# Kernel optimization log

Measured on AMD Instinct MI355X. Metric: run time of the kernel, lower is better.

Reference implementation:

```python
import jax, jax.numpy as jnp
from jax import lax
import numpy as np

B, T, I, H, L, O = 64, 256, 128, 1024, 3, 2


def setup_inputs() -> dict:
    key = jax.random.key(0)
    ks = jax.random.split(key, 12)
    std = 1.0 / np.sqrt(H)
    u = lambda k, shape: jax.random.uniform(k, shape, jnp.float32, -std, std)
    return {
        "x": jax.random.normal(ks[0], (B, T, I), jnp.float32),
        # layer 0 cell (input_size -> hidden)
        "wx0": u(ks[1], (H, I)), "bx0": u(ks[2], (H,)),
        "wh0": u(ks[3], (H, H)), "bh0": u(ks[4], (H,)),
        # layers 1..L-1 cells (hidden -> hidden), stacked
        "wx": u(ks[5], (L - 1, H, H)), "bx": u(ks[6], (L - 1, H)),
        "wh": u(ks[7], (L - 1, H, H)), "bh": u(ks[8], (L - 1, H)),
        # final fc
        "fcw": u(ks[9], (O, H)), "fcb": u(ks[10], (O,)),
    }


def reference(x, wx0, bx0, wh0, bh0, wx, bx, wh, bh, fcw, fcb):
    b = x.shape[0]
    n_rest = wx.shape[0]  # num_layers - 1
    h0 = jnp.zeros((n_rest + 1, b, wh0.shape[0]), x.dtype)
    xT = jnp.swapaxes(x, 0, 1)  # [T, B, I]

    def step(hs, xt):
        new = []
        h = jnp.tanh(xt @ wx0.T + bx0 + hs[0] @ wh0.T + bh0)
        new.append(h)
        for l in range(n_rest):  # small fixed layer loop
            h = jnp.tanh(new[l] @ wx[l].T + bx[l] + hs[l + 1] @ wh[l].T + bh[l])
            new.append(h)
        return jnp.stack(new), None

    hs_final, _ = lax.scan(step, h0, xT)
    # original collects per-step top-layer outputs but only uses the last one
    return hs_final[-1] @ fcw.T + fcb  # [B, O]
```

## Files before the change

### kernel.cpp

```cpp
#include <hip/hip_runtime.h>


typedef __attribute__((ext_vector_type(8))) short short8;
typedef __attribute__((ext_vector_type(4))) float float4v;

#define DEVFN static __device__ __forceinline__

#define GLD(dst, ptr) \
  asm volatile("global_load_dwordx4 %0, %1, off sc1" : "=v"(dst) : "v"(ptr))
#define GST16(ptr, val) \
  asm volatile("global_store_dwordx4 %0, %1, off sc1" :: "v"(ptr), "v"(val) : "memory")
#define GDRAIN() do { asm volatile("s_waitcnt vmcnt(0)" ::: "memory"); \
                      __builtin_amdgcn_sched_barrier(0); } while (0)

DEVFN unsigned short f2bf(float f) {
  unsigned int u = __float_as_uint(f);
  u += 0x7FFFu + ((u >> 16) & 1u);
  return (unsigned short)(u >> 16);
}
DEVFN float bf2f(unsigned short h) { return __uint_as_float(((unsigned int)h) << 16); }

DEVFN void spin_ge(int* p, int want) {
  while (__hip_atomic_load(p, __ATOMIC_RELAXED, __HIP_MEMORY_SCOPE_AGENT) < want)
    __builtin_amdgcn_s_sleep(1);
}

namespace rnncfg {
constexpr int  TT = 256, HH = 1024;
constexpr long WELEMS = 1024L * 1152 + 2L * 1024 * 2048;
constexpr long XELEMS = 64L * 256 * 128;
constexpr long HELEMS = 3L * 4 * 64 * HH;
constexpr long PELEMS = 48L * 4 * 4096;

constexpr long OFF_WHI  = 0;
constexpr long OFF_WLO  = OFF_WHI + WELEMS * 2;
constexpr long OFF_XHI  = OFF_WLO + WELEMS * 2;
constexpr long OFF_XLO  = OFF_XHI + XELEMS * 2;
constexpr long OFF_HHI  = OFF_XLO + XELEMS * 2;
constexpr long OFF_HLO  = OFF_HHI + HELEMS * 2;
constexpr long OFF_BIAS = OFF_HLO + HELEMS * 2;
constexpr long OFF_CNT  = OFF_BIAS + 3L * HH * 4;
constexpr long N_CNT    = 768 + 48L * 256;
constexpr long OFF_PART = OFF_CNT + N_CNT * 4;
constexpr long WS_NEED  = OFF_PART + PELEMS * 4;

constexpr int SMEM_BYTES = 4 * 64 * 65 * 4;
}

__global__ __launch_bounds__(256) void rnn_prep_kernel(
    const float* __restrict__ x,
    const float* __restrict__ wx0, const float* __restrict__ bx0,
    const float* __restrict__ wh0, const float* __restrict__ bh0,
    const float* __restrict__ wx,  const float* __restrict__ bx,
    const float* __restrict__ wh,  const float* __restrict__ bh,
    char* __restrict__ ws)
{
  using namespace rnncfg;
  unsigned short* WHI = (unsigned short*)(ws + OFF_WHI);
  unsigned short* WLO = (unsigned short*)(ws + OFF_WLO);
  unsigned short* XHI = (unsigned short*)(ws + OFF_XHI);
  unsigned short* XLO = (unsigned short*)(ws + OFF_XLO);
  float* BIAS = (float*)(ws + OFF_BIAS);
  int*   CNT  = (int*)(ws + OFF_CNT);
  const long i0 = (long)blockIdx.x * blockDim.x + threadIdx.x;
  const long st = (long)gridDim.x * blockDim.x;

  for (long i = i0; i < N_CNT; i += st) CNT[i] = 0;

  for (long i = i0; i < 3 * HH; i += st) {
    int l = (int)(i >> 10), n = (int)(i & 1023);
    BIAS[i] = (l == 0) ? (bx0[n] + bh0[n]) : (bx[(l - 1) * HH + n] + bh[(l - 1) * HH + n]);
  }
  for (long i = i0; i < XELEMS; i += st) {
    float v = x[i];
    unsigned short h = f2bf(v);
    XHI[i] = h; XLO[i] = f2bf(v - bf2f(h));
  }
  for (long i = i0; i < WELEMS; i += st) {
    long j = i; int n, k; float v;
    if (j < 1179648L) {
      n = (int)(j / 1152); k = (int)(j % 1152);
      v = (k < 128) ? wx0[n * 128 + k] : wh0[(long)n * 1024 + (k - 128)];
    } else if (j < 3276800L) {
      j -= 1179648L; n = (int)(j / 2048); k = (int)(j % 2048);
      v = (k < 1024) ? wx[(long)n * 1024 + k] : wh[(long)n * 1024 + (k - 1024)];
    } else {
      j -= 3276800L; n = (int)(j / 2048); k = (int)(j % 2048);
      v = (k < 1024) ? wx[1048576L + (long)n * 1024 + k]
                     : wh[1048576L + (long)n * 1024 + (k - 1024)];
    }
    unsigned short h = f2bf(v);
    WHI[i] = h; WLO[i] = f2bf(v - bf2f(h));
  }
}

#define MFMA(a, b, c) __builtin_amdgcn_mfma_f32_16x16x32_bf16((a), (b), (c), 0, 0, 0)

template<int L>
DEVFN void run_block(char* __restrict__ ws, int tid, int g, int cg, int q,
                     float* __restrict__ pbuf, int* __restrict__ sFlag)
{
  using namespace rnncfg;
  constexpr long LWOFF = (L == 0) ? 0L : ((L == 1) ? 1179648L : 3276800L);
  constexpr int  KL    = (L == 0) ? 1152 : 2048;

  const unsigned short* WHI = (const unsigned short*)(ws + OFF_WHI);
  const unsigned short* WLO = (const unsigned short*)(ws + OFF_WLO);
  const unsigned short* XHI = (const unsigned short*)(ws + OFF_XHI);
  const unsigned short* XLO = (const unsigned short*)(ws + OFF_XLO);
  unsigned short* HHI = (unsigned short*)(ws + OFF_HHI);
  unsigned short* HLO = (unsigned short*)(ws + OFF_HLO);
  const float* BIAS = (const float*)(ws + OFF_BIAS);
  int* READY = (int*)(ws + OFF_CNT);
  int* ARR   = READY + 768;
  float* PART = (float*)(ws + OFF_PART);

  const int lane = tid & 63, wv = tid >> 6;
  const int rowb = lane & 15;
  const int kof  = (lane >> 4) * 8;
  const int n0   = cg * 64;

  short8 bh[4][4], bl[4][4];
  short8 bxh[4], bxl[4];
  if constexpr (L == 0) {
#pragma unroll
    for (int nt = 0; nt < 4; ++nt) {
      const long wr = LWOFF + (long)(n0 + nt * 16 + rowb) * KL;
      if (q == 0) { bxh[nt] = *(const short8*)(WHI + wr + wv * 32 + kof);
                    bxl[nt] = *(const short8*)(WLO + wr + wv * 32 + kof); }
#pragma unroll
      for (int j = 0; j < 2; ++j) {
        const int kc = 128 + q * 256 + wv * 64 + j * 32 + kof;
        bh[nt][j] = *(const short8*)(WHI + wr + kc);
        bl[nt][j] = *(const short8*)(WLO + wr + kc);
      }
    }
  } else {
#pragma unroll
    for (int nt = 0; nt < 4; ++nt) {
      const long wr = LWOFF + (long)(n0 + nt * 16 + rowb) * KL;
#pragma unroll
      for (int ks = 0; ks < 4; ++ks) {
        const int kc = q * 512 + wv * 128 + ks * 32 + kof;
        bh[nt][ks] = *(const short8*)(WHI + wr + kc);
        bl[nt][ks] = *(const short8*)(WLO + wr + kc);
      }
    }
  }

  float* myP = PART + (long)(g * 4 + q) * 4096;
  int* arrp = ARR + g * 256;

  for (int t = 0; t < TT; ++t) {
    if (tid == 0) {
      if (t > 0) spin_ge(&READY[L * 256 + t - 1], 16);
      if (L > 0) spin_ge(&READY[(L - 1) * 256 + t], 16);
    }
    __syncthreads();

    const unsigned short* selfH = HHI + (long)(L * 4 + ((t - 1) & 3)) * 65536;
    const unsigned short* selfL = HLO + (long)(L * 4 + ((t - 1) & 3)) * 65536;

    float4v acc[4][4];
#pragma unroll
    for (int mt = 0; mt < 4; ++mt)
#pragma unroll
      for (int nt = 0; nt < 4; ++nt) acc[mt][nt] = (float4v){0.f, 0.f, 0.f, 0.f};

    if constexpr (L == 0) {
      short8 xh[4], xl[4], ah[4][2], al[4][2];
      if (q == 0) {
#pragma unroll
        for (int mt = 0; mt < 4; ++mt) {
          const long xo = ((long)(mt * 16 + rowb) * 256 + t) * 128 + wv * 32 + kof;
          xh[mt] = *(const short8*)(XHI + xo);
          xl[mt] = *(const short8*)(XLO + xo);
        }
      }
      if (t > 0) {
        const int kb = q * 256 + wv * 64 + kof;
#pragma unroll
        for (int mt = 0; mt < 4; ++mt) {
          const int ao = (mt * 16 + rowb) * 1024 + kb;
#pragma unroll
          for (int j = 0; j < 2; ++j) { GLD(ah[mt][j], selfH + ao + j * 32);
                                        GLD(al[mt][j], selfL + ao + j * 32); }
        }
      }
      GDRAIN();
      if (q == 0) {
#pragma unroll
        for (int mt = 0; mt < 4; ++mt)
#pragma unroll
          for (int nt = 0; nt < 4; ++nt) {
            acc[mt][nt] = MFMA(xh[mt], bxh[nt], acc[mt][nt]);
            acc[mt][nt] = MFMA(xh[mt], bxl[nt], acc[mt][nt]);
            acc[mt][nt] = MFMA(xl[mt], bxh[nt], acc[mt][nt]);
          }
      }
      if (t > 0) {
#pragma unroll
        for (int j = 0; j < 2; ++j)
#pragma unroll
          for (int mt = 0; mt < 4; ++mt)
#pragma unroll
            for (int nt = 0; nt < 4; ++nt) {
              acc[mt][nt] = MFMA(ah[mt][j], bh[nt][j], acc[mt][nt]);
              acc[mt][nt] = MFMA(ah[mt][j], bl[nt][j], acc[mt][nt]);
              acc[mt][nt] = MFMA(al[mt][j], bh[nt][j], acc[mt][nt]);
            }
      }
    } else {
      if (!(t == 0 && q >= 2)) {
        const unsigned short* AH = (q < 2)
            ? HHI + (long)((L - 1) * 4 + (t & 3)) * 65536 : selfH;
        const unsigned short* AL = (q < 2)
            ? HLO + (long)((L - 1) * 4 + (t & 3)) * 65536 : selfL;
        const int kb = (q & 1) * 512 + wv * 128 + kof;
        short8 ah[4][4], al[4][4];
#pragma unroll
        for (int mt = 0; mt < 4; ++mt) {
          const int ao = (mt * 16 + rowb) * 1024 + kb;
#pragma unroll
          for (int ks = 0; ks < 4; ++ks) { GLD(ah[mt][ks], AH + ao + ks * 32);
                                           GLD(al[mt][ks], AL + ao + ks * 32); }
        }
        GDRAIN();
#pragma unroll
        for (int ks = 0; ks < 4; ++ks)
#pragma unroll
          for (int mt = 0; mt < 4; ++mt)
#pragma unroll
            for (int nt = 0; nt < 4; ++nt) {
              acc[mt][nt] = MFMA(ah[mt][ks], bh[nt][ks], acc[mt][nt]);
              acc[mt][nt] = MFMA(ah[mt][ks], bl[nt][ks], acc[mt][nt]);
              acc[mt][nt] = MFMA(al[mt][ks], bh[nt][ks], acc[mt][nt]);
            }
      }
    }

#pragma unroll
    for (int mt = 0; mt < 4; ++mt)
#pragma unroll
      for (int nt = 0; nt < 4; ++nt)
#pragma unroll
        for (int r = 0; r < 4; ++r)
          pbuf[wv * 4160 + (mt * 16 + (lane >> 4) * 4 + r) * 65 + nt * 16 + rowb]
              = acc[mt][nt][r];
    __syncthreads();

    {
      const int prow = tid >> 2, pc0 = (tid & 3) * 16;
#pragma unroll
      for (int cq = 0; cq < 4; ++cq) {
        float4v s = *(const float4v*)(pbuf +        prow * 65 + pc0 + cq * 4);
        s += *(const float4v*)(pbuf + 4160 + prow * 65 + pc0 + cq * 4);
        s += *(const float4v*)(pbuf + 8320 + prow * 65 + pc0 + cq * 4);
        s += *(const float4v*)(pbuf + 12480 + prow * 65 + pc0 + cq * 4);
        GST16(myP + prow * 64 + pc0 + cq * 4, s);
      }
    }
    GDRAIN();
    __syncthreads();
    if (tid == 0) {
      const int old = __hip_atomic_fetch_add(&arrp[t], 1, __ATOMIC_RELAXED,
                                             __HIP_MEMORY_SCOPE_AGENT);
      *sFlag = (old == 3);
    }
    __syncthreads();

    if (*sFlag) {
      if (tid == 0 && L < 2 && t >= 4) spin_ge(&READY[(L + 1) * 256 + t - 4], 16);
      __syncthreads();

      const int prow = tid >> 2, pc0 = (tid & 3) * 16;
      const float* P0 = PART + (long)(g * 4) * 4096 + prow * 64 + pc0;
      float4v pa[4][4];
#pragma unroll
      for (int qq = 0; qq < 4; ++qq)
#pragma unroll
        for (int cq = 0; cq < 4; ++cq)
          GLD(pa[qq][cq], P0 + qq * 4096 + cq * 4);
      GDRAIN();

      unsigned short* dH = HHI + (long)(L * 4 + (t & 3)) * 65536 + prow * 1024 + n0 + pc0;
      unsigned short* dL = HLO + (long)(L * 4 + (t & 3)) * 65536 + prow * 1024 + n0 + pc0;
      short8 vh[2], vl[2];
#pragma unroll
      for (int cq = 0; cq < 4; ++cq) {
        const float4v s = (pa[0][cq] + pa[1][cq]) + (pa[2][cq] + pa[3][cq]);
#pragma unroll
        for (int j = 0; j < 4; ++j) {
          const float v = tanhf(s[j] + BIAS[L * 1024 + n0 + pc0 + cq * 4 + j]);
          const unsigned short hh = f2bf(v);
          vh[cq >> 1][(cq & 1) * 4 + j] = (short)hh;
          vl[cq >> 1][(cq & 1) * 4 + j] = (short)f2bf(v - bf2f(hh));
        }
      }
      GST16(dH, vh[0]); GST16(dH + 8, vh[1]);
      GST16(dL, vl[0]); GST16(dL + 8, vl[1]);
      GDRAIN();
      __syncthreads();
      if (tid == 0)
        __hip_atomic_fetch_add(&READY[L * 256 + t], 1, __ATOMIC_RELAXED,
                               __HIP_MEMORY_SCOPE_AGENT);
    }
  }
}

__global__ __launch_bounds__(256, 1) void rnn_pipeline_kernel(
    char* __restrict__ ws, const float* __restrict__ fcw,
    const float* __restrict__ fcb, float* __restrict__ out)
{
  using namespace rnncfg;
  extern __shared__ float pbuf[];
  __shared__ int sFlag;
  const int tid = threadIdx.x, bid = blockIdx.x;

  const int xcd = bid & 7, s = bid >> 3;
  const int q = s & 3, gslot = s >> 2;
  const int g = gslot * 8 + xcd;
  const int layer = g >> 4, cg = g & 15;

  if (layer == 0)      run_block<0>(ws, tid, g, cg, q, pbuf, &sFlag);
  else if (layer == 1) run_block<1>(ws, tid, g, cg, q, pbuf, &sFlag);
  else                 run_block<2>(ws, tid, g, cg, q, pbuf, &sFlag);

  if (bid == 0) {
    int* READY = (int*)(ws + OFF_CNT);
    if (tid == 0) spin_ge(&READY[2 * 256 + 255], 16);
    __syncthreads();
    if (tid < 128) {
      const unsigned short* HHI = (const unsigned short*)(ws + OFF_HHI);
      const unsigned short* HLO = (const unsigned short*)(ws + OFF_HLO);
      const int bb = tid >> 1, o = tid & 1;
      const unsigned short* hH = HHI + (long)(2 * 4 + 3) * 65536 + (long)bb * 1024;
      const unsigned short* hL = HLO + (long)(2 * 4 + 3) * 65536 + (long)bb * 1024;
      const float* w = fcw + o * 1024;
      float sum = fcb[o];
      for (int n = 0; n < 1024; n += 32) {
        short8 vh[4], vl[4];
#pragma unroll
        for (int qq = 0; qq < 4; ++qq) { GLD(vh[qq], hH + n + qq * 8);
                                         GLD(vl[qq], hL + n + qq * 8); }
        GDRAIN();
#pragma unroll
        for (int qq = 0; qq < 4; ++qq)
#pragma unroll
          for (int j = 0; j < 8; ++j)
            sum += (bf2f((unsigned short)vh[qq][j]) + bf2f((unsigned short)vl[qq][j]))
                   * w[n + qq * 8 + j];
      }
      out[bb * 2 + o] = sum;
    }
  }
}

extern "C" void kernel_launch(void* const* d_in, const int* in_sizes, int n_in,
                              void* d_out, int out_size, void* d_ws, size_t ws_size,
                              hipStream_t stream)
{
  using namespace rnncfg;
  const float* x   = (const float*)d_in[0];
  const float* wx0 = (const float*)d_in[1];
  const float* bx0 = (const float*)d_in[2];
  const float* wh0 = (const float*)d_in[3];
  const float* bh0 = (const float*)d_in[4];
  const float* wx  = (const float*)d_in[5];
  const float* bx  = (const float*)d_in[6];
  const float* wh  = (const float*)d_in[7];
  const float* bh  = (const float*)d_in[8];
  const float* fcw = (const float*)d_in[9];
  const float* fcb = (const float*)d_in[10];
  char* ws = (char*)d_ws;
  float* out = (float*)d_out;

  if (ws_size < (size_t)WS_NEED) return;

  hipFuncSetAttribute(reinterpret_cast<const void*>(rnn_pipeline_kernel),
                      hipFuncAttributeMaxDynamicSharedMemorySize, SMEM_BYTES);

  rnn_prep_kernel<<<dim3(1024), dim3(256), 0, stream>>>(
      x, wx0, bx0, wh0, bh0, wx, bx, wh, bh, ws);
  rnn_pipeline_kernel<<<dim3(192), dim3(256), SMEM_BYTES, stream>>>(
      ws, fcw, fcb, out);
}
```

Measured before the change: 4.128 ms.

## Replace per-layer step barriers with fine-grained per-column-group ready flags

```diff
diff --git a/kernel.cpp b/kernel.cpp
--- a/kernel.cpp
+++ b/kernel.cpp
@@ -23,6 +23,16 @@
 DEVFN void spin_ge(int* p, int want) {
   while (__hip_atomic_load(p, __ATOMIC_RELAXED, __HIP_MEMORY_SCOPE_AGENT) < want)
     __builtin_amdgcn_s_sleep(1);
+}
+
+DEVFN void spin_flags(int* base, int n) {
+  const int tid = threadIdx.x;
+  if (tid < n) {
+    int* p = base + tid;
+    while (__hip_atomic_load(p, __ATOMIC_RELAXED, __HIP_MEMORY_SCOPE_AGENT) < 1)
+      __builtin_amdgcn_s_sleep(1);
+  }
+  __syncthreads();
 }
 
 namespace rnncfg {
@@ -40,7 +50,7 @@
 constexpr long OFF_HLO  = OFF_HHI + HELEMS * 2;
 constexpr long OFF_BIAS = OFF_HLO + HELEMS * 2;
 constexpr long OFF_CNT  = OFF_BIAS + 3L * HH * 4;
-constexpr long N_CNT    = 768 + 48L * 256;
+constexpr long N_CNT    = 768 + 48L * 256 + 3L * 256 * 16;
 constexpr long OFF_PART = OFF_CNT + N_CNT * 4;
 constexpr long WS_NEED  = OFF_PART + PELEMS * 4;
 
@@ -111,8 +121,9 @@
   unsigned short* HHI = (unsigned short*)(ws + OFF_HHI);
   unsigned short* HLO = (unsigned short*)(ws + OFF_HLO);
   const float* BIAS = (const float*)(ws + OFF_BIAS);
-  int* READY = (int*)(ws + OFF_CNT);
-  int* ARR   = READY + 768;
+  int* READY  = (int*)(ws + OFF_CNT);
+  int* ARR    = READY + 768;
+  int* READY2 = ARR + 48 * 256;
   float* PART = (float*)(ws + OFF_PART);
 
   const int lane = tid & 63, wv = tid >> 6;
@@ -152,15 +163,6 @@
   int* arrp = ARR + g * 256;
 
   for (int t = 0; t < TT; ++t) {
-    if (tid == 0) {
-      if (t > 0) spin_ge(&READY[L * 256 + t - 1], 16);
-      if (L > 0) spin_ge(&READY[(L - 1) * 256 + t], 16);
-    }
-    __syncthreads();
-
-    const unsigned short* selfH = HHI + (long)(L * 4 + ((t - 1) & 3)) * 65536;
-    const unsigned short* selfL = HLO + (long)(L * 4 + ((t - 1) & 3)) * 65536;
-
     float4v acc[4][4];
 #pragma unroll
     for (int mt = 0; mt < 4; ++mt)
@@ -168,27 +170,14 @@
       for (int nt = 0; nt < 4; ++nt) acc[mt][nt] = (float4v){0.f, 0.f, 0.f, 0.f};
 
     if constexpr (L == 0) {
-      short8 xh[4], xl[4], ah[4][2], al[4][2];
       if (q == 0) {
+        short8 xh[4], xl[4];
 #pragma unroll
         for (int mt = 0; mt < 4; ++mt) {
           const long xo = ((long)(mt * 16 + rowb) * 256 + t) * 128 + wv * 32 + kof;
           xh[mt] = *(const short8*)(XHI + xo);
           xl[mt] = *(const short8*)(XLO + xo);
         }
-      }
-      if (t > 0) {
-        const int kb = q * 256 + wv * 64 + kof;
-#pragma unroll
-        for (int mt = 0; mt < 4; ++mt) {
-          const int ao = (mt * 16 + rowb) * 1024 + kb;
-#pragma unroll
-          for (int j = 0; j < 2; ++j) { GLD(ah[mt][j], selfH + ao + j * 32);
-                                        GLD(al[mt][j], selfL + ao + j * 32); }
-        }
-      }
-      GDRAIN();
-      if (q == 0) {
 #pragma unroll
         for (int mt = 0; mt < 4; ++mt)
 #pragma unroll
@@ -199,6 +188,19 @@
           }
       }
       if (t > 0) {
+        spin_flags(&READY2[(0 * 256 + t - 1) * 16 + q * 4], 4);
+        const unsigned short* SH = HHI + (long)(((t - 1) & 3)) * 65536;
+        const unsigned short* SL = HLO + (long)(((t - 1) & 3)) * 65536;
+        const int kb = q * 256 + wv * 64 + kof;
+        short8 ah[4][2], al[4][2];
+#pragma unroll
+        for (int mt = 0; mt < 4; ++mt) {
+          const int ao = (mt * 16 + rowb) * 1024 + kb;
+#pragma unroll
+          for (int j = 0; j < 2; ++j) { GLD(ah[mt][j], SH + ao + j * 32);
+                                        GLD(al[mt][j], SL + ao + j * 32); }
+        }
+        GDRAIN();
 #pragma unroll
         for (int j = 0; j < 2; ++j)
 #pragma unroll
@@ -211,12 +213,11 @@
             }
       }
     } else {
-      if (!(t == 0 && q >= 2)) {
-        const unsigned short* AH = (q < 2)
-            ? HHI + (long)((L - 1) * 4 + (t & 3)) * 65536 : selfH;
-        const unsigned short* AL = (q < 2)
-            ? HLO + (long)((L - 1) * 4 + (t & 3)) * 65536 : selfL;
-        const int kb = (q & 1) * 512 + wv * 128 + kof;
+      if (q < 2) {
+        spin_flags(&READY2[((L - 1) * 256 + t) * 16 + q * 8], 8);
+        const unsigned short* AH = HHI + (long)((L - 1) * 4 + (t & 3)) * 65536;
+        const unsigned short* AL = HLO + (long)((L - 1) * 4 + (t & 3)) * 65536;
+        const int kb = q * 512 + wv * 128 + kof;
         short8 ah[4][4], al[4][4];
 #pragma unroll
         for (int mt = 0; mt < 4; ++mt) {
@@ -236,6 +237,30 @@
               acc[mt][nt] = MFMA(ah[mt][ks], bl[nt][ks], acc[mt][nt]);
               acc[mt][nt] = MFMA(al[mt][ks], bh[nt][ks], acc[mt][nt]);
             }
+      } else if (t > 0) {
+        spin_flags(&READY2[(L * 256 + t - 1) * 16 + (q - 2) * 8], 8);
+        const unsigned short* AH = HHI + (long)(L * 4 + ((t - 1) & 3)) * 65536;
+        const unsigned short* AL = HLO + (long)(L * 4 + ((t - 1) & 3)) * 65536;
+        const int kb = (q - 2) * 512 + wv * 128 + kof;
+        short8 ah[4][4], al[4][4];
+#pragma unroll
+        for (int mt = 0; mt < 4; ++mt) {
+          const int ao = (mt * 16 + rowb) * 1024 + kb;
+#pragma unroll
+          for (int ks = 0; ks < 4; ++ks) { GLD(ah[mt][ks], AH + ao + ks * 32);
+                                           GLD(al[mt][ks], AL + ao + ks * 32); }
+        }
+        GDRAIN();
+#pragma unroll
+        for (int ks = 0; ks < 4; ++ks)
+#pragma unroll
+          for (int mt = 0; mt < 4; ++mt)
+#pragma unroll
+            for (int nt = 0; nt < 4; ++nt) {
+              acc[mt][nt] = MFMA(ah[mt][ks], bh[nt][ks], acc[mt][nt]);
+              acc[mt][nt] = MFMA(ah[mt][ks], bl[nt][ks], acc[mt][nt]);
+              acc[mt][nt] = MFMA(al[mt][ks], bh[nt][ks], acc[mt][nt]);
+            }
       }
     }
 
@@ -249,13 +274,18 @@
               = acc[mt][nt][r];
     __syncthreads();
 
+    if (t > 0) {
+      if (tid == 0) spin_ge(&READY2[(L * 256 + t - 1) * 16 + cg], 1);
+      __syncthreads();
+    }
+
     {
       const int prow = tid >> 2, pc0 = (tid & 3) * 16;
 #pragma unroll
       for (int cq = 0; cq < 4; ++cq) {
-        float4v s = *(const float4v*)(pbuf +        prow * 65 + pc0 + cq * 4);
-        s += *(const float4v*)(pbuf + 4160 + prow * 65 + pc0 + cq * 4);
-        s += *(const float4v*)(pbuf + 8320 + prow * 65 + pc0 + cq * 4);
+        float4v s = *(const float4v*)(pbuf +         prow * 65 + pc0 + cq * 4);
+        s += *(const float4v*)(pbuf +  4160 + prow * 65 + pc0 + cq * 4);
+        s += *(const float4v*)(pbuf +  8320 + prow * 65 + pc0 + cq * 4);
         s += *(const float4v*)(pbuf + 12480 + prow * 65 + pc0 + cq * 4);
         GST16(myP + prow * 64 + pc0 + cq * 4, s);
       }
@@ -301,9 +331,12 @@
       GST16(dL, vl[0]); GST16(dL + 8, vl[1]);
       GDRAIN();
       __syncthreads();
-      if (tid == 0)
+      if (tid == 0) {
+        __hip_atomic_store(&READY2[(L * 256 + t) * 16 + cg], 1,
+                           __ATOMIC_RELAXED, __HIP_MEMORY_SCOPE_AGENT);
         __hip_atomic_fetch_add(&READY[L * 256 + t], 1, __ATOMIC_RELAXED,
                                __HIP_MEMORY_SCOPE_AGENT);
+      }
     }
   }
 }
```

New measurement: 4.021 ms. -2.6%, faster.
